# Performance work log

Hardware: AMD Instinct MI355X
Metric: run time of the kernel (lower is better)

The kernel has to match this reference:

```python
import jax, jax.numpy as jnp
import numpy as np

N_RAYS = 65536   # 256x256 image
N_PTS = 128      # samples per ray
FEAT = 3         # RGB
FAR_DELTA = 1e10 # sentinel delta for last sample, as in the torch module


def setup_inputs() -> dict:
    key = jax.random.key(0)
    k1, k2, k3 = jax.random.split(key, 3)
    # depths along each ray must be increasing (deltas computed by diff)
    depth_values = jnp.sort(
        jax.random.uniform(k1, (N_RAYS, N_PTS), jnp.float32, 2.0, 6.0), axis=-1)
    density = jax.random.uniform(k2, (N_RAYS, N_PTS), jnp.float32)  # non-negative
    feature = jax.random.uniform(k3, (N_RAYS, N_PTS, FEAT), jnp.float32)
    return {"depth_values": depth_values, "density": density, "feature": feature}


def reference(depth_values, density, feature):
    n_rays, n_pts = depth_values.shape
    # deltas: consecutive depth differences, huge value appended for last bin
    deltas = jnp.concatenate(
        [depth_values[:, 1:] - depth_values[:, :-1],
         jnp.full((n_rays, 1), FAR_DELTA, depth_values.dtype)], axis=-1)
    tau = density * deltas                              # [n_rays, n_pts]
    # transmittance T_i = exp(-sum_{j<i} tau_j) (exclusive cumsum in log space)
    log_T = -jnp.concatenate(
        [jnp.zeros((n_rays, 1), tau.dtype), jnp.cumsum(tau[:, :-1], axis=-1)],
        axis=-1)
    weights = jnp.exp(log_T) * (1.0 - jnp.exp(-tau))    # [n_rays, n_pts]
    feat_out = jnp.einsum('np,npf->nf', weights, feature)         # [n_rays, F]
    depth_out = jnp.sum(weights * depth_values, axis=-1, keepdims=True)
    return jnp.concatenate([feat_out, depth_out], axis=-1)        # [n_rays, F+1]
```

## Files before the change

### kernel.cpp

```cpp
#include <hip/hip_runtime.h>

#define N_RAYS 65536
#define N_PTS  128
#define FAR_DELTA 1e10f

#define BLOCK   256
#define NBLOCKS 2048
#define NWAVES  (NBLOCKS * (BLOCK / 64))
#define NPAIRS  (N_RAYS / 2)
#define NPASS   (NPAIRS / NWAVES)

__global__ __launch_bounds__(BLOCK, 6) void volrend_kernel(
    const float* __restrict__ depth,
    const float* __restrict__ density,
    const float* __restrict__ feature,
    float* __restrict__ out)
{
    const int lane = threadIdx.x & 63;
    const int sl   = lane & 31;
    const int g    = (int)blockIdx.x * (BLOCK / 64) + (threadIdx.x >> 6);

    float4 d, rho, f0, f1, f2;
    float4 pd, pr, pf0, pf1, pf2;

#define LOADP(p_, D_, R_, F0_, F1_, F2_)                                      \
    do {                                                                      \
        size_t rb_ = (size_t)(2 * (p_)) * N_PTS + 4 * lane;                   \
        D_ = *(const float4*)(depth + rb_);                                   \
        R_ = *(const float4*)(density + rb_);                                 \
        const float* fp_ = feature + (size_t)(2 * (p_)) * (N_PTS * 3)         \
                         + 12 * lane;                                         \
        F0_ = *(const float4*)(fp_);                                          \
        F1_ = *(const float4*)(fp_ + 4);                                      \
        F2_ = *(const float4*)(fp_ + 8);                                      \
    } while (0)

    LOADP(g, d, rho, f0, f1, f2);

#pragma unroll
    for (int p = 0; p < NPASS; ++p) {
        if (p + 1 < NPASS)
            LOADP((p + 1) * NWAVES + g, pd, pr, pf0, pf1, pf2);

        float nx = __shfl_down(d.x, 1);
        float t0 = rho.x * (d.y - d.x);
        float t1 = rho.y * (d.z - d.y);
        float t2 = rho.z * (d.w - d.z);
        float t3 = rho.w * ((sl == 31) ? FAR_DELTA : (nx - d.w));
        float q1 = t0, q2 = q1 + t1, q3 = q2 + t2, tot = q3 + t3;

        float e = __shfl_up(tot, 1);
        if (sl == 0) e = 0.0f;
        #pragma unroll
        for (int off = 1; off < 32; off <<= 1) {
            float u = __shfl_up(e, off);
            if (sl >= off) e += u;
        }

        float T0 = __expf(-e);
        float T1 = __expf(-(e + q1));
        float T2 = __expf(-(e + q2));
        float T3 = __expf(-(e + q3));
        float T4 = __expf(-(e + tot));
        float w0 = T0 - T1, w1 = T1 - T2, w2 = T2 - T3, w3 = T3 - T4;

        float a3 = w0 * d.x  + w1 * d.y  + w2 * d.z  + w3 * d.w;
        float a0 = w0 * f0.x + w1 * f0.w + w2 * f1.z + w3 * f2.y;
        float a1 = w0 * f0.y + w1 * f1.x + w2 * f1.w + w3 * f2.z;
        float a2 = w0 * f0.z + w1 * f1.y + w2 * f2.x + w3 * f2.w;

        #pragma unroll
        for (int off = 16; off > 0; off >>= 1) {
            a0 += __shfl_xor(a0, off);
            a1 += __shfl_xor(a1, off);
            a2 += __shfl_xor(a2, off);
            a3 += __shfl_xor(a3, off);
        }
        if (sl == 0) {
            int ray = 2 * (p * NWAVES + g) + (lane >> 5);
            *(float4*)(out + (size_t)ray * 4) = make_float4(a0, a1, a2, a3);
        }

        d = pd; rho = pr; f0 = pf0; f1 = pf1; f2 = pf2;
    }
#undef LOADP
}

extern "C" void kernel_launch(void* const* d_in, const int* in_sizes, int n_in,
                              void* d_out, int out_size, void* d_ws, size_t ws_size,
                              hipStream_t stream) {
    const float* depth   = (const float*)d_in[0];
    const float* density = (const float*)d_in[1];
    const float* feature = (const float*)d_in[2];
    float* out = (float*)d_out;

    dim3 grid(NBLOCKS);
    dim3 block(BLOCK);
    volrend_kernel<<<grid, block, 0, stream>>>(depth, density, feature, out);
}
```

Baseline: 194.6 us.

## Stream inputs through LDS with async global_load_lds double buffering

Replaces register prefetching with direct global-to-LDS async loads (global_load_lds, 16 bytes per lane) into a per-wave double buffer. Two passes are kept in flight, synchronised with hand-written vmcnt/lgkmcnt waits, and the grid is halved so each wave handles more passes. The feature loads become fully coalesced 256-float chunks that are de-interleaved from LDS. The aim is deeper memory-level parallelism and lower register pressure on this bandwidth-bound kernel. The cost is added LDS traffic, and the hand-counted vmcnt values are fragile: the output stores also count as vector memory operations.

Result: no change. 194.5 us (-0.1%).

```diff
diff --git a/kernel.cpp b/kernel.cpp
--- a/kernel.cpp
+++ b/kernel.cpp
@@ -5,42 +5,60 @@
 #define FAR_DELTA 1e10f
 
 #define BLOCK   256
-#define NBLOCKS 2048
+#define NBLOCKS 1024
 #define NWAVES  (NBLOCKS * (BLOCK / 64))
 #define NPAIRS  (N_RAYS / 2)
-#define NPASS   (NPAIRS / NWAVES)
+#define NP      (NPAIRS / NWAVES)
 
-__global__ __launch_bounds__(BLOCK, 6) void volrend_kernel(
+__global__ __launch_bounds__(BLOCK) void volrend_kernel(
     const float* __restrict__ depth,
     const float* __restrict__ density,
     const float* __restrict__ feature,
     float* __restrict__ out)
 {
-    const int lane = threadIdx.x & 63;
+    __shared__ float4 sbuf[4][2][5 * 64];
+
+    const int tid  = threadIdx.x;
+    const int w    = tid >> 6;
+    const int lane = tid & 63;
     const int sl   = lane & 31;
-    const int g    = (int)blockIdx.x * (BLOCK / 64) + (threadIdx.x >> 6);
+    const int g    = (int)blockIdx.x * (BLOCK / 64) + w;
 
-    float4 d, rho, f0, f1, f2;
-    float4 pd, pr, pf0, pf1, pf2;
+#define GLD(gp_, lp_)                                                         \
+    __builtin_amdgcn_global_load_lds(                                         \
+        (const __attribute__((address_space(1))) void*)(gp_),                 \
+        (__attribute__((address_space(3))) void*)(lp_), 16, 0, 0)
 
-#define LOADP(p_, D_, R_, F0_, F1_, F2_)                                      \
+#define ISSUE(p_, b_)                                                         \
     do {                                                                      \
-        size_t rb_ = (size_t)(2 * (p_)) * N_PTS + 4 * lane;                   \
-        D_ = *(const float4*)(depth + rb_);                                   \
-        R_ = *(const float4*)(density + rb_);                                 \
-        const float* fp_ = feature + (size_t)(2 * (p_)) * (N_PTS * 3)         \
-                         + 12 * lane;                                         \
-        F0_ = *(const float4*)(fp_);                                          \
-        F1_ = *(const float4*)(fp_ + 4);                                      \
-        F2_ = *(const float4*)(fp_ + 8);                                      \
+        float4* wb_ = &sbuf[w][b_][0];                                        \
+        GLD(depth   + (size_t)(p_) * 256 + 4 * lane, wb_);                    \
+        GLD(density + (size_t)(p_) * 256 + 4 * lane, wb_ + 64);               \
+        const float* fp_ = feature + (size_t)(p_) * 768 + 4 * lane;           \
+        GLD(fp_,       wb_ + 128);                                            \
+        GLD(fp_ + 256, wb_ + 192);                                            \
+        GLD(fp_ + 512, wb_ + 256);                                            \
     } while (0)
 
-    LOADP(g, d, rho, f0, f1, f2);
+    ISSUE(g, 0);
+    ISSUE(NWAVES + g, 1);
 
 #pragma unroll
-    for (int p = 0; p < NPASS; ++p) {
-        if (p + 1 < NPASS)
-            LOADP((p + 1) * NWAVES + g, pd, pr, pf0, pf1, pf2);
+    for (int p = 0; p < NP; ++p) {
+        if      (p == 0)      asm volatile("s_waitcnt vmcnt(5)" ::: "memory");
+        else if (p == 1)      asm volatile("s_waitcnt vmcnt(6)" ::: "memory");
+        else if (p < NP - 1)  asm volatile("s_waitcnt vmcnt(7)" ::: "memory");
+        else                  asm volatile("s_waitcnt vmcnt(2)" ::: "memory");
+
+        const float4* wb = &sbuf[w][p & 1][0];
+        float4 d   = wb[lane];
+        float4 rho = wb[64 + lane];
+        float4 f0  = wb[128 + 3 * lane];
+        float4 f1  = wb[129 + 3 * lane];
+        float4 f2  = wb[130 + 3 * lane];
+
+        asm volatile("s_waitcnt lgkmcnt(0)" ::: "memory");
+        if (p + 2 < NP) ISSUE((p + 2) * NWAVES + g, p & 1);
 
         float nx = __shfl_down(d.x, 1);
         float t0 = rho.x * (d.y - d.x);
@@ -80,10 +98,9 @@
             int ray = 2 * (p * NWAVES + g) + (lane >> 5);
             *(float4*)(out + (size_t)ray * 4) = make_float4(a0, a1, a2, a3);
         }
-
-        d = pd; rho = pr; f0 = pf0; f1 = pf1; f2 = pf2;
     }
-#undef LOADP
+#undef ISSUE
+#undef GLD
 }
 
 extern "C" void kernel_launch(void* const* d_in, const int* in_sizes, int n_in,
```
